# Kernel tuning notes

Measured on AMD Instinct MI355X. Metric: run time of the kernel, lower is better.

Reference implementation:

```python
import jax, jax.numpy as jnp
import numpy as np

NUM_GENS = 1024
N = 8388608

def setup_inputs() -> dict:
    key = jax.random.key(0)
    k1, k2, k3, k4, k5, k6, k7, k8 = jax.random.split(key, 8)
    return {
        "x_gen": jax.random.randint(k1, (N,), 0, NUM_GENS, dtype=jnp.int64 if jax.config.jax_enable_x64 else jnp.int32),
        "x_ix": jax.random.randint(k2, (N,), 0, NUM_GENS, dtype=jnp.int64 if jax.config.jax_enable_x64 else jnp.int32),
        "x_max_clock_speed": jax.random.normal(k3, (N,), dtype=jnp.float32),
        "x_max_tdp": jax.random.normal(k4, (N,), dtype=jnp.float32),
        "gen_map": jax.random.normal(k5, (NUM_GENS,), dtype=jnp.float32),
        "b": jax.random.normal(k6, (), dtype=jnp.float32),
        "c": jax.random.normal(k7, (), dtype=jnp.float32),
        "d": jax.random.normal(k8, (), dtype=jnp.float32),
    }

def reference(x_gen, x_ix, x_max_clock_speed, x_max_tdp, gen_map, b, c, d):
    # sum(one_hot(x_gen, G) * gen_map, 1) is mathematically gen_map[x_gen]
    gathered = jnp.take(gen_map, x_gen, axis=0)  # [N]
    return gathered + c * x_max_clock_speed + d * x_max_tdp
```

## Files before the change

kernel.cpp:

```cpp
#include <hip/hip_runtime.h>


#define NUM_GENS 1024

__global__ __launch_bounds__(256)
void Model_64364379898151_kernel(const int* __restrict__ x_gen,
                                 const float* __restrict__ x_clock,
                                 const float* __restrict__ x_tdp,
                                 const float* __restrict__ gen_map,
                                 const float* __restrict__ c_ptr,
                                 const float* __restrict__ d_ptr,
                                 float* __restrict__ out,
                                 int n_vec)
{
    __shared__ float s_map[NUM_GENS];
    for (int i = threadIdx.x; i < NUM_GENS; i += 256)
        s_map[i] = gen_map[i];
    __syncthreads();

    const float c = c_ptr[0];
    const float d = d_ptr[0];

    int vid = blockIdx.x * 256 + threadIdx.x;
    if (vid >= n_vec) return;

    const int4   g  = ((const int4*)  x_gen  )[vid];
    const float4 cs = ((const float4*)x_clock)[vid];
    const float4 td = ((const float4*)x_tdp  )[vid];

    float4 o;
    o.x = s_map[g.x] + c * cs.x + d * td.x;
    o.y = s_map[g.y] + c * cs.y + d * td.y;
    o.z = s_map[g.z] + c * cs.z + d * td.z;
    o.w = s_map[g.w] + c * cs.w + d * td.w;

    ((float4*)out)[vid] = o;
}

extern "C" void kernel_launch(void* const* d_in, const int* in_sizes, int n_in,
                              void* d_out, int out_size, void* d_ws, size_t ws_size,
                              hipStream_t stream) {
    const int*   x_gen   = (const int*)  d_in[0];
    const float* x_clock = (const float*)d_in[2];
    const float* x_tdp   = (const float*)d_in[3];
    const float* gen_map = (const float*)d_in[4];
    const float* c_ptr   = (const float*)d_in[6];
    const float* d_ptr   = (const float*)d_in[7];
    float* out = (float*)d_out;

    const int n = in_sizes[0];
    const int n_vec = n / 4;
    const int block = 256;
    const int grid = (n_vec + block - 1) / block;

    Model_64364379898151_kernel<<<grid, block, 0, stream>>>(
        x_gen, x_clock, x_tdp, gen_map, c_ptr, d_ptr, out, n_vec);
}
```

Measured before the change: 165.2 us.

## Use persistent grid-stride loop with 4-way unrolled vector loads

Replaces the one-block-per-1024-elements launch with a fixed grid of 2048 blocks that loop over the data with a grid stride, processing four float4 groups per iteration to raise memory-level parallelism. The shared-memory table fill becomes a single float4 load per thread, and it happens once per persistent block instead of once per small block. This trades occupancy flexibility for fewer redundant table loads and more outstanding loads per thread. It assumes NUM_GENS equals 4*BLOCK.

Result: no change. 166.3 us (+0.7%).

```diff
diff --git a/kernel.cpp b/kernel.cpp
--- a/kernel.cpp
+++ b/kernel.cpp
@@ -2,8 +2,11 @@
 
 
 #define NUM_GENS 1024
+#define BLOCK 256
+#define GRID 2048
+#define UNROLL 4
 
-__global__ __launch_bounds__(256)
+__global__ __launch_bounds__(BLOCK)
 void Model_64364379898151_kernel(const int* __restrict__ x_gen,
                                  const float* __restrict__ x_clock,
                                  const float* __restrict__ x_tdp,
@@ -14,27 +17,66 @@
                                  int n_vec)
 {
     __shared__ float s_map[NUM_GENS];
-    for (int i = threadIdx.x; i < NUM_GENS; i += 256)
-        s_map[i] = gen_map[i];
+    ((float4*)s_map)[threadIdx.x] = ((const float4*)gen_map)[threadIdx.x];
     __syncthreads();
 
     const float c = c_ptr[0];
     const float d = d_ptr[0];
 
-    int vid = blockIdx.x * 256 + threadIdx.x;
-    if (vid >= n_vec) return;
+    const int stride = GRID * BLOCK;
+    int idx = blockIdx.x * BLOCK + threadIdx.x;
 
-    const int4   g  = ((const int4*)  x_gen  )[vid];
-    const float4 cs = ((const float4*)x_clock)[vid];
-    const float4 td = ((const float4*)x_tdp  )[vid];
+    const int4*   g4 = (const int4*)  x_gen;
+    const float4* c4 = (const float4*)x_clock;
+    const float4* t4 = (const float4*)x_tdp;
+    float4*       o4 = (float4*)      out;
 
-    float4 o;
-    o.x = s_map[g.x] + c * cs.x + d * td.x;
-    o.y = s_map[g.y] + c * cs.y + d * td.y;
-    o.z = s_map[g.z] + c * cs.z + d * td.z;
-    o.w = s_map[g.w] + c * cs.w + d * td.w;
+    for (int base = idx; base < n_vec; base += UNROLL * stride) {
+        const int i1 = base + stride;
+        const int i2 = base + 2 * stride;
+        const int i3 = base + 3 * stride;
 
-    ((float4*)out)[vid] = o;
+        if (i3 < n_vec) {
+            int4   g0 = g4[base], g1 = g4[i1], g2 = g4[i2], g3 = g4[i3];
+            float4 cs0 = c4[base], cs1 = c4[i1], cs2 = c4[i2], cs3 = c4[i3];
+            float4 td0 = t4[base], td1 = t4[i1], td2 = t4[i2], td3 = t4[i3];
+
+            float4 o0, o1, o2, o3;
+            o0.x = s_map[g0.x] + c * cs0.x + d * td0.x;
+            o0.y = s_map[g0.y] + c * cs0.y + d * td0.y;
+            o0.z = s_map[g0.z] + c * cs0.z + d * td0.z;
+            o0.w = s_map[g0.w] + c * cs0.w + d * td0.w;
+            o1.x = s_map[g1.x] + c * cs1.x + d * td1.x;
+            o1.y = s_map[g1.y] + c * cs1.y + d * td1.y;
+            o1.z = s_map[g1.z] + c * cs1.z + d * td1.z;
+            o1.w = s_map[g1.w] + c * cs1.w + d * td1.w;
+            o2.x = s_map[g2.x] + c * cs2.x + d * td2.x;
+            o2.y = s_map[g2.y] + c * cs2.y + d * td2.y;
+            o2.z = s_map[g2.z] + c * cs2.z + d * td2.z;
+            o2.w = s_map[g2.w] + c * cs2.w + d * td2.w;
+            o3.x = s_map[g3.x] + c * cs3.x + d * td3.x;
+            o3.y = s_map[g3.y] + c * cs3.y + d * td3.y;
+            o3.z = s_map[g3.z] + c * cs3.z + d * td3.z;
+            o3.w = s_map[g3.w] + c * cs3.w + d * td3.w;
+
+            o4[base] = o0; o4[i1] = o1; o4[i2] = o2; o4[i3] = o3;
+        } else {
+            for (int k = 0; k < UNROLL; ++k) {
+                int i = base + k * stride;
+                if (i < n_vec) {
+                    int4   g  = g4[i];
+                    float4 cs = c4[i];
+                    float4 td = t4[i];
+                    float4 o;
+                    o.x = s_map[g.x] + c * cs.x + d * td.x;
+                    o.y = s_map[g.y] + c * cs.y + d * td.y;
+                    o.z = s_map[g.z] + c * cs.z + d * td.z;
+                    o.w = s_map[g.w] + c * cs.w + d * td.w;
+                    o4[i] = o;
+                }
+            }
+        }
+    }
 }
 
 extern "C" void kernel_launch(void* const* d_in, const int* in_sizes, int n_in,
@@ -50,9 +92,7 @@
 
     const int n = in_sizes[0];
     const int n_vec = n / 4;
-    const int block = 256;
-    const int grid = (n_vec + block - 1) / block;
 
-    Model_64364379898151_kernel<<<grid, block, 0, stream>>>(
+    Model_64364379898151_kernel<<<GRID, BLOCK, 0, stream>>>(
         x_gen, x_clock, x_tdp, gen_map, c_ptr, d_ptr, out, n_vec);
 }
```

## Use fixed grid-stride kernel with batched nontemporal loads and stores

Applied to the files above, without the earlier changes.

Launches a fixed 1024-block grid in which each thread handles eight float4 groups. All 24 vector loads are issued before any compute, and results are written with nontemporal stores. The gen_map table is staged into shared memory with one float4 per thread, which amortizes that per-block cost over far fewer blocks. The aim is more memory-level parallelism and less launch and per-block overhead for this bandwidth-bound gather-FMA. The cost is higher register pressure, plus a specialised fast path that only runs when n_vec exactly equals eight times the grid stride.

After: 157.4 us. 4.7% less time.

```diff
diff --git a/kernel.cpp b/kernel.cpp
--- a/kernel.cpp
+++ b/kernel.cpp
@@ -2,8 +2,24 @@
 
 
 #define NUM_GENS 1024
+#define BLOCK 256
+#define GRID 1024
+#define UNROLL 4
 
-__global__ __launch_bounds__(256)
+typedef float nfloat4 __attribute__((ext_vector_type(4)));
+typedef int   nint4   __attribute__((ext_vector_type(4)));
+
+__device__ __forceinline__ nfloat4 stage_compute(const float* s_map, float c, float d,
+                                                 nint4 g, nfloat4 a, nfloat4 b) {
+    nfloat4 o;
+    o.x = s_map[g.x] + c * a.x + d * b.x;
+    o.y = s_map[g.y] + c * a.y + d * b.y;
+    o.z = s_map[g.z] + c * a.z + d * b.z;
+    o.w = s_map[g.w] + c * a.w + d * b.w;
+    return o;
+}
+
+__global__ __launch_bounds__(BLOCK, 4)
 void Model_64364379898151_kernel(const int* __restrict__ x_gen,
                                  const float* __restrict__ x_clock,
                                  const float* __restrict__ x_tdp,
@@ -14,27 +30,71 @@
                                  int n_vec)
 {
     __shared__ float s_map[NUM_GENS];
-    for (int i = threadIdx.x; i < NUM_GENS; i += 256)
-        s_map[i] = gen_map[i];
+    ((float4*)s_map)[threadIdx.x] = ((const float4*)gen_map)[threadIdx.x];
     __syncthreads();
 
     const float c = c_ptr[0];
     const float d = d_ptr[0];
 
-    int vid = blockIdx.x * 256 + threadIdx.x;
-    if (vid >= n_vec) return;
+    const int stride = GRID * BLOCK;
+    const int idx = blockIdx.x * BLOCK + threadIdx.x;
 
-    const int4   g  = ((const int4*)  x_gen  )[vid];
-    const float4 cs = ((const float4*)x_clock)[vid];
-    const float4 td = ((const float4*)x_tdp  )[vid];
+    const nint4*   g4 = (const nint4*)  x_gen;
+    const nfloat4* c4 = (const nfloat4*)x_clock;
+    const nfloat4* t4 = (const nfloat4*)x_tdp;
+    nfloat4*       o4 = (nfloat4*)      out;
 
-    float4 o;
-    o.x = s_map[g.x] + c * cs.x + d * td.x;
-    o.y = s_map[g.y] + c * cs.y + d * td.y;
-    o.z = s_map[g.z] + c * cs.z + d * td.z;
-    o.w = s_map[g.w] + c * cs.w + d * td.w;
+    if (n_vec == 8 * stride) {
+        const int j0 = idx;
+        const int j1 = idx + 1 * stride;
+        const int j2 = idx + 2 * stride;
+        const int j3 = idx + 3 * stride;
+        const int j4 = idx + 4 * stride;
+        const int j5 = idx + 5 * stride;
+        const int j6 = idx + 6 * stride;
+        const int j7 = idx + 7 * stride;
 
-    ((float4*)out)[vid] = o;
+        nint4   gA0 = __builtin_nontemporal_load(g4 + j0);
+        nint4   gA1 = __builtin_nontemporal_load(g4 + j1);
+        nint4   gA2 = __builtin_nontemporal_load(g4 + j2);
+        nint4   gA3 = __builtin_nontemporal_load(g4 + j3);
+        nfloat4 aA0 = __builtin_nontemporal_load(c4 + j0);
+        nfloat4 aA1 = __builtin_nontemporal_load(c4 + j1);
+        nfloat4 aA2 = __builtin_nontemporal_load(c4 + j2);
+        nfloat4 aA3 = __builtin_nontemporal_load(c4 + j3);
+        nfloat4 bA0 = __builtin_nontemporal_load(t4 + j0);
+        nfloat4 bA1 = __builtin_nontemporal_load(t4 + j1);
+        nfloat4 bA2 = __builtin_nontemporal_load(t4 + j2);
+        nfloat4 bA3 = __builtin_nontemporal_load(t4 + j3);
+        nint4   gB0 = __builtin_nontemporal_load(g4 + j4);
+        nint4   gB1 = __builtin_nontemporal_load(g4 + j5);
+        nint4   gB2 = __builtin_nontemporal_load(g4 + j6);
+        nint4   gB3 = __builtin_nontemporal_load(g4 + j7);
+        nfloat4 aB0 = __builtin_nontemporal_load(c4 + j4);
+        nfloat4 aB1 = __builtin_nontemporal_load(c4 + j5);
+        nfloat4 aB2 = __builtin_nontemporal_load(c4 + j6);
+        nfloat4 aB3 = __builtin_nontemporal_load(c4 + j7);
+        nfloat4 bB0 = __builtin_nontemporal_load(t4 + j4);
+        nfloat4 bB1 = __builtin_nontemporal_load(t4 + j5);
+        nfloat4 bB2 = __builtin_nontemporal_load(t4 + j6);
+        nfloat4 bB3 = __builtin_nontemporal_load(t4 + j7);
+
+        __builtin_nontemporal_store(stage_compute(s_map, c, d, gA0, aA0, bA0), o4 + j0);
+        __builtin_nontemporal_store(stage_compute(s_map, c, d, gA1, aA1, bA1), o4 + j1);
+        __builtin_nontemporal_store(stage_compute(s_map, c, d, gA2, aA2, bA2), o4 + j2);
+        __builtin_nontemporal_store(stage_compute(s_map, c, d, gA3, aA3, bA3), o4 + j3);
+        __builtin_nontemporal_store(stage_compute(s_map, c, d, gB0, aB0, bB0), o4 + j4);
+        __builtin_nontemporal_store(stage_compute(s_map, c, d, gB1, aB1, bB1), o4 + j5);
+        __builtin_nontemporal_store(stage_compute(s_map, c, d, gB2, aB2, bB2), o4 + j6);
+        __builtin_nontemporal_store(stage_compute(s_map, c, d, gB3, aB3, bB3), o4 + j7);
+    } else {
+        for (int i = idx; i < n_vec; i += stride) {
+            nint4   g  = __builtin_nontemporal_load(g4 + i);
+            nfloat4 cs = __builtin_nontemporal_load(c4 + i);
+            nfloat4 td = __builtin_nontemporal_load(t4 + i);
+            __builtin_nontemporal_store(stage_compute(s_map, c, d, g, cs, td), o4 + i);
+        }
+    }
 }
 
 extern "C" void kernel_launch(void* const* d_in, const int* in_sizes, int n_in,
@@ -50,9 +110,7 @@
 
     const int n = in_sizes[0];
     const int n_vec = n / 4;
-    const int block = 256;
-    const int grid = (n_vec + block - 1) / block;
 
-    Model_64364379898151_kernel<<<grid, block, 0, stream>>>(
+    Model_64364379898151_kernel<<<GRID, BLOCK, 0, stream>>>(
         x_gen, x_clock, x_tdp, gen_map, c_ptr, d_ptr, out, n_vec);
 }
```
